# Performance work log

Measured on AMD Instinct MI355X. Metric: run time of the kernel, lower is better.

Reference implementation:

```python
import jax, jax.numpy as jnp
import numpy as np

N_NODES = 50000


def _gcn_conv(x, W, b, src, dst, n):
    # PyG GCNConv: h = x @ W, symmetric-normalized aggregation, then + bias.
    h = x @ W  # [N, out]
    deg = jax.ops.segment_sum(jnp.ones_like(dst, dtype=h.dtype), dst, num_segments=n)
    dinv = jnp.where(deg > 0, jax.lax.rsqrt(jnp.maximum(deg, 1e-12)), 0.0)
    norm = dinv[src] * dinv[dst]  # [E]
    msg = h[src] * norm[:, None]  # gather + scale, [E, out]
    out = jax.ops.segment_sum(msg, dst, num_segments=n)
    return out + b


def setup_inputs() -> dict:
    key = jax.random.key(0)
    ks = jax.random.split(key, 8)
    d_in, d_h, d_out = 256, 256, 128
    E = 800000
    x = jax.random.normal(ks[0], (N_NODES, d_in), dtype=jnp.float32)
    edge_index = jax.random.randint(ks[1], (2, E), 0, N_NODES, dtype=jnp.int64)
    def glorot(k, shape):
        lim = np.sqrt(6.0 / (shape[0] + shape[1]))
        return jax.random.uniform(k, shape, jnp.float32, -lim, lim)
    return {
        "x": x,
        "edge_index": edge_index,
        "W1": glorot(ks[2], (d_in, d_h)), "b1": jnp.zeros((d_h,), jnp.float32),
        "W2": glorot(ks[3], (d_h, d_h)), "b2": jnp.zeros((d_h,), jnp.float32),
        "W3": glorot(ks[4], (d_h, d_out)), "b3": jnp.zeros((d_out,), jnp.float32),
    }


def reference(x, edge_index, W1, b1, W2, b2, W3, b3):
    n = x.shape[0]
    # add self-loops once (PyG GCNConv default add_self_loops=True)
    loop = jnp.arange(n, dtype=edge_index.dtype)
    src = jnp.concatenate([edge_index[0], loop])
    dst = jnp.concatenate([edge_index[1], loop])
    h = _gcn_conv(x, W1, b1, src, dst, n)
    h = jax.nn.relu(h)  # dropout is identity in eval mode
    h = _gcn_conv(h, W2, b2, src, dst, n)
    h = jax.nn.relu(h)
    h = _gcn_conv(h, W3, b3, src, dst, n)
    return h
```

## Files before the change

kernel.cpp:

```cpp
#include <hip/hip_runtime.h>
#include <stdint.h>

typedef short v8s __attribute__((ext_vector_type(8)));
typedef float v4f __attribute__((ext_vector_type(4)));
typedef float v2f __attribute__((ext_vector_type(2)));

__device__ inline float bf2f(unsigned short h) {
    union { unsigned u; float f; } c; c.u = ((unsigned)h) << 16; return c.f;
}
__device__ inline unsigned short f2bf(float f) {
    union { float f; unsigned u; } c; c.f = f;
    unsigned u = c.u;
    unsigned r = (u + 0x7FFFu + ((u >> 16) & 1u)) >> 16;
    return (unsigned short)r;
}
__device__ inline void gl_lds16(const unsigned short* g, unsigned short* l) {
    __builtin_amdgcn_global_load_lds(
        (const __attribute__((address_space(1))) unsigned int*)(g),
        (__attribute__((address_space(3))) unsigned int*)(l), 16, 0, 0);
}

__global__ void k_pre1(const int* __restrict__ dst, int E,
                       int* __restrict__ cnt, int* __restrict__ seq,
                       const float* __restrict__ x, unsigned short* __restrict__ A,
                       int n, int mpad,
                       const float* __restrict__ W1, const float* __restrict__ W2,
                       const float* __restrict__ W3, unsigned short* __restrict__ Wt,
                       int gE, int gX) {
    int b = blockIdx.x;
    if (b < gE) {
        int e = b * 256 + threadIdx.x;
        if (e < E) seq[e] = atomicAdd(&cnt[dst[e]], 1);
    } else if (b < gE + gX) {
        int g = (b - gE) * 256 + threadIdx.x;
        int total = mpad * 64;
        if (g >= total) return;
        int row = g >> 6;
        float4 v;
        if (row < n) v = ((const float4*)x)[(size_t)g];
        else v = make_float4(0.f, 0.f, 0.f, 0.f);
        ushort4 o;
        o.x = f2bf(v.x); o.y = f2bf(v.y); o.z = f2bf(v.z); o.w = f2bf(v.w);
        ((ushort4*)A)[(size_t)g] = o;
    } else {
        int idx = (b - gE - gX) * 256 + threadIdx.x;
        const float* W; int base, N;
        if (idx < 65536)       { W = W1; base = 0;      N = 256; }
        else if (idx < 131072) { W = W2; base = 65536;  N = 256; }
        else                   { W = W3; base = 131072; N = 128; }
        int loc = idx - base;
        int nn = loc >> 8;
        int k = loc & 255;
        Wt[idx] = f2bf(W[(size_t)k * N + nn]);
    }
}

__global__ void k_scan1(const int* __restrict__ cnt, int n, int* __restrict__ incl,
                        int* __restrict__ bsum) {
    __shared__ int sm[256];
    int t = threadIdx.x;
    int i = blockIdx.x * 256 + t;
    int v = (i < n) ? cnt[i] : 0;
    sm[t] = v; __syncthreads();
    for (int off = 1; off < 256; off <<= 1) {
        int add = (t >= off) ? sm[t - off] : 0;
        __syncthreads();
        sm[t] += add;
        __syncthreads();
    }
    if (i < n) incl[i] = sm[t];
    if (t == 255) bsum[blockIdx.x] = sm[255];
}

__global__ void k_scan23(const int* __restrict__ cnt, int n,
                         const int* __restrict__ bsum,
                         int* __restrict__ rs, float* __restrict__ dinv) {
    __shared__ int red[256];
    int t = threadIdx.x;
    int acc = 0;
    for (int j = t; j < (int)blockIdx.x; j += 256) acc += bsum[j];
    red[t] = acc; __syncthreads();
    for (int s = 128; s > 0; s >>= 1) {
        if (t < s) red[t] += red[t + s];
        __syncthreads();
    }
    int boff = red[0];
    int i = blockIdx.x * 256 + t;
    if (i < n) {
        int c = cnt[i];
        rs[i] = rs[i] + boff - c;
        dinv[i] = rsqrtf((float)(c + 1));
    }
}

__global__ void k_scatter2(const int* __restrict__ src, const int* __restrict__ dst,
                           const int* __restrict__ seq, int E,
                           const int* __restrict__ rs, int* __restrict__ col) {
    int e = blockIdx.x * 256 + threadIdx.x;
    if (e < E) col[rs[dst[e]] + seq[e]] = src[e];
}

__launch_bounds__(256, 3)
__global__ void k_gemm(const unsigned short* __restrict__ A,
                       const unsigned short* __restrict__ Wt,
                       unsigned short* __restrict__ Hs,
                       const float* __restrict__ dinv, int n, int N) {
    __shared__ unsigned short sA[2][128 * 32];
    __shared__ unsigned short sB[2][128 * 32];
    const int t = threadIdx.x;
    const int lane = t & 63;
    const int wave = t >> 6;
    const int wm = wave >> 1, wn = wave & 1;
    const int m0 = blockIdx.x * 128;
    const int n0 = blockIdx.y * 128;

    v4f acc[4][4];
#pragma unroll
    for (int i = 0; i < 4; i++)
#pragma unroll
        for (int j = 0; j < 4; j++)
#pragma unroll
            for (int r = 0; r < 4; r++) acc[i][j][r] = 0.f;

    const int c0 = t, c1 = t + 256;
    const int r0 = c0 >> 2, kc0 = (c0 & 3) * 8;
    const int r1 = c1 >> 2, kc1 = (c1 & 3) * 8;
    const size_t aBase0 = (size_t)(m0 + r0) * 256 + kc0;
    const size_t aBase1 = (size_t)(m0 + r1) * 256 + kc1;
    const size_t bBase0 = (size_t)(n0 + r0) * 256 + kc0;
    const size_t bBase1 = (size_t)(n0 + r1) * 256 + kc1;

    const int q = lane >> 4;
    const int lm = lane & 15;

    gl_lds16(A + aBase0, &sA[0][c0 * 8]);
    gl_lds16(A + aBase1, &sA[0][c1 * 8]);
    gl_lds16(Wt + bBase0, &sB[0][c0 * 8]);
    gl_lds16(Wt + bBase1, &sB[0][c1 * 8]);

    for (int k0 = 0; k0 < 256; k0 += 32) {
        const int cur = (k0 >> 5) & 1;
        __syncthreads();
        if (k0 < 224) {
            const int nxt = cur ^ 1;
            gl_lds16(A + aBase0 + k0 + 32, &sA[nxt][c0 * 8]);
            gl_lds16(A + aBase1 + k0 + 32, &sA[nxt][c1 * 8]);
            gl_lds16(Wt + bBase0 + k0 + 32, &sB[nxt][c0 * 8]);
            gl_lds16(Wt + bBase1 + k0 + 32, &sB[nxt][c1 * 8]);
        }

        v8s afr[4], bfr[4];
#pragma unroll
        for (int i = 0; i < 4; i++) {
            int r = wm * 64 + i * 16 + lm;
            afr[i] = *(const v8s*)&sA[cur][r * 32 + q * 8];
        }
#pragma unroll
        for (int j = 0; j < 4; j++) {
            int nn = wn * 64 + j * 16 + lm;
            bfr[j] = *(const v8s*)&sB[cur][nn * 32 + q * 8];
        }
#pragma unroll
        for (int i = 0; i < 4; i++)
#pragma unroll
            for (int j = 0; j < 4; j++)
                acc[i][j] = __builtin_amdgcn_mfma_f32_16x16x32_bf16(afr[i], bfr[j],
                                                                    acc[i][j], 0, 0, 0);
    }

#pragma unroll
    for (int i = 0; i < 4; i++) {
        int mbase = m0 + wm * 64 + i * 16 + q * 4;
#pragma unroll
        for (int r = 0; r < 4; r++) {
            int m = mbase + r;
            float s = (m < n) ? dinv[m] : 0.f;
#pragma unroll
            for (int j = 0; j < 4; j++) {
                int colI = n0 + wn * 64 + j * 16 + lm;
                Hs[(size_t)m * N + colI] = f2bf(acc[i][j][r] * s);
            }
        }
    }
}

template <int D, bool RELU, bool F32OUT>
__launch_bounds__(256, 8)
__global__ void k_agg(const unsigned short* __restrict__ Hs,
                      const int* __restrict__ rs, const int* __restrict__ cnt,
                      const int* __restrict__ col, const float* __restrict__ dinv,
                      const float* __restrict__ bias,
                      unsigned short* __restrict__ outb, float* __restrict__ outf,
                      int n, int nzero) {
    constexpr int LPN = D / 8;
    constexpr int NPG = 64 / LPN;
    const int lane = threadIdx.x & 63;
    const int i = blockIdx.x * 4 + (threadIdx.x >> 6);
    if (i >= n) return;
    const int g = lane / LPN;
    const int cl = lane % LPN;

    v2f acc[4];
#pragma unroll
    for (int k = 0; k < 4; k++) acc[k] = (v2f){0.f, 0.f};

    auto accq = [&](unsigned u, int k) {
        union { unsigned uu; float f; } lo, hi;
        lo.uu = u << 16;
        hi.uu = u & 0xffff0000u;
        v2f t; t[0] = lo.f; t[1] = hi.f;
        acc[k] += t;
    };
    auto acc16 = [&](uint4 q) { accq(q.x, 0); accq(q.y, 1); accq(q.z, 2); accq(q.w, 3); };

    const unsigned short* base = Hs + cl * 8;
    const int s = rs[i], deg = cnt[i];
    const int T = deg + 1;
    const int Tpad = (T + NPG - 1) & ~(NPG - 1);

    for (int b = 0; b < Tpad; b += 64) {
        int t = b + lane;
        int v;
        if (t == 0) v = i;
        else if (t <= deg) v = col[s + t - 1];
        else v = nzero;
        int lim = min(64, Tpad - b);
        int t2 = 0;
        for (; t2 + 4 * NPG <= lim; t2 += 4 * NPG) {
            int c0 = __shfl(v, t2 + 0 * NPG + g);
            int c1 = __shfl(v, t2 + 1 * NPG + g);
            int c2 = __shfl(v, t2 + 2 * NPG + g);
            int c3 = __shfl(v, t2 + 3 * NPG + g);
            uint4 q0 = *(const uint4*)(base + (size_t)c0 * D);
            uint4 q1 = *(const uint4*)(base + (size_t)c1 * D);
            uint4 q2 = *(const uint4*)(base + (size_t)c2 * D);
            uint4 q3 = *(const uint4*)(base + (size_t)c3 * D);
            acc16(q0); acc16(q1); acc16(q2); acc16(q3);
        }
        for (; t2 + NPG <= lim; t2 += NPG) {
            int c0 = __shfl(v, t2 + g);
            uint4 q0 = *(const uint4*)(base + (size_t)c0 * D);
            acc16(q0);
        }
    }

#pragma unroll
    for (int off = LPN; off < 64; off <<= 1) {
#pragma unroll
        for (int k = 0; k < 4; k++) {
            acc[k][0] += __shfl_xor(acc[k][0], off);
            acc[k][1] += __shfl_xor(acc[k][1], off);
        }
    }

    if (g == 0) {
        float di = dinv[i];
        float o[8];
#pragma unroll
        for (int k = 0; k < 4; k++) {
            o[2 * k + 0] = di * acc[k][0] + bias[cl * 8 + 2 * k + 0];
            o[2 * k + 1] = di * acc[k][1] + bias[cl * 8 + 2 * k + 1];
        }
        if (RELU) {
#pragma unroll
            for (int k = 0; k < 8; k++) o[k] = fmaxf(o[k], 0.f);
        }
        if constexpr (F32OUT) {
            float* p = outf + (size_t)i * D + cl * 8;
            *(float4*)p = make_float4(o[0], o[1], o[2], o[3]);
            *(float4*)(p + 4) = make_float4(o[4], o[5], o[6], o[7]);
        } else {
            uint4 q;
            q.x = ((unsigned)f2bf(o[1]) << 16) | f2bf(o[0]);
            q.y = ((unsigned)f2bf(o[3]) << 16) | f2bf(o[2]);
            q.z = ((unsigned)f2bf(o[5]) << 16) | f2bf(o[4]);
            q.w = ((unsigned)f2bf(o[7]) << 16) | f2bf(o[6]);
            *(uint4*)(outb + (size_t)i * D + cl * 8) = q;
        }
    }
}

extern "C" void kernel_launch(void* const* d_in, const int* in_sizes, int n_in,
                              void* d_out, int out_size, void* d_ws, size_t ws_size,
                              hipStream_t stream) {
    const float* x  = (const float*)d_in[0];
    const int*   ei = (const int*)d_in[1];
    const float* W1 = (const float*)d_in[2];
    const float* b1 = (const float*)d_in[3];
    const float* W2 = (const float*)d_in[4];
    const float* b2 = (const float*)d_in[5];
    const float* W3 = (const float*)d_in[6];
    const float* b3 = (const float*)d_in[7];

    const int n = in_sizes[0] / 256;
    const int E = in_sizes[1] / 2;
    const int mpad = ((n + 127) / 128) * 128;

    char* ws = (char*)d_ws;
    size_t off = 0;
    auto alloc = [&](size_t bytes) -> void* {
        void* p = ws + off;
        off += (bytes + 255) & ~(size_t)255;
        return p;
    };
    int* cnt      = (int*)alloc((size_t)n * 4);
    int* rs       = (int*)alloc((size_t)n * 4);
    float* dinv   = (float*)alloc((size_t)n * 4);
    int* bsum     = (int*)alloc(256 * 4);
    int* seq      = (int*)alloc((size_t)E * 4);
    int* col      = (int*)alloc((size_t)E * 4);
    unsigned short* Wt = (unsigned short*)alloc((size_t)163840 * 2);
    unsigned short* W1t = Wt;
    unsigned short* W2t = Wt + 65536;
    unsigned short* W3t = Wt + 131072;
    unsigned short* bufA = (unsigned short*)alloc((size_t)mpad * 256 * 2);
    unsigned short* bufB = (unsigned short*)alloc((size_t)mpad * 256 * 2);
    (void)ws_size; (void)n_in; (void)out_size;

    const int* srcp = ei;
    const int* dstp = ei + E;
    const int gE = (E + 255) / 256;
    const int gN = (n + 255) / 256;
    const int gX = (mpad * 64 + 255) / 256;
    const int gW = 640;

    hipMemsetAsync(cnt, 0, (size_t)n * 4, stream);

    k_pre1<<<gE + gX + gW, 256, 0, stream>>>(dstp, E, cnt, seq, x, bufA, n, mpad,
                                             W1, W2, W3, Wt, gE, gX);
    k_scan1<<<gN, 256, 0, stream>>>(cnt, n, rs, bsum);
    k_scan23<<<gN, 256, 0, stream>>>(cnt, n, bsum, rs, dinv);
    k_scatter2<<<gE, 256, 0, stream>>>(srcp, dstp, seq, E, rs, col);

    const int gAgg = (n + 3) / 4;
    dim3 gg1(mpad / 128, 2);
    k_gemm<<<gg1, 256, 0, stream>>>(bufA, W1t, bufB, dinv, n, 256);
    k_agg<256, true, false><<<gAgg, 256, 0, stream>>>(bufB, rs, cnt, col, dinv, b1,
                                                      bufA, nullptr, n, n);
    k_gemm<<<gg1, 256, 0, stream>>>(bufA, W2t, bufB, dinv, n, 256);
    k_agg<256, true, false><<<gAgg, 256, 0, stream>>>(bufB, rs, cnt, col, dinv, b2,
                                                      bufA, nullptr, n, n);
    dim3 gg3(mpad / 128, 1);
    k_gemm<<<gg3, 256, 0, stream>>>(bufA, W3t, bufB, dinv, n, 128);
    k_agg<128, false, true><<<gAgg, 256, 0, stream>>>(bufB, rs, cnt, col, dinv, b3,
                                                      nullptr, (float*)d_out, n, n);
}
```

Measured before the change: 364.3 us.

## Shrink GEMM tile to 64x128, drop LDS double buffering, raise occupancy

The GEMM block tile shrinks from 128x128 to 64x128, with each wave computing a 64x32 slice. The two-stage LDS double buffer is replaced by a single buffer guarded by two barriers per k-step, and launch bounds rise to 6 blocks per SM. The aim is to double the grid size and raise occupancy so latency is hidden by more resident waves rather than by software prefetch. The cost is lower data reuse per block (each W tile is fetched twice as often), extra barriers, and no overlap of loads with MFMA inside a block.

```diff
diff --git a/kernel.cpp b/kernel.cpp
--- a/kernel.cpp
+++ b/kernel.cpp
@@ -100,84 +100,70 @@
     if (e < E) col[rs[dst[e]] + seq[e]] = src[e];
 }
 
-__launch_bounds__(256, 3)
+__launch_bounds__(256, 6)
 __global__ void k_gemm(const unsigned short* __restrict__ A,
                        const unsigned short* __restrict__ Wt,
                        unsigned short* __restrict__ Hs,
                        const float* __restrict__ dinv, int n, int N) {
-    __shared__ unsigned short sA[2][128 * 32];
-    __shared__ unsigned short sB[2][128 * 32];
+    __shared__ unsigned short sA[64 * 32];
+    __shared__ unsigned short sB[128 * 32];
     const int t = threadIdx.x;
     const int lane = t & 63;
-    const int wave = t >> 6;
-    const int wm = wave >> 1, wn = wave & 1;
-    const int m0 = blockIdx.x * 128;
+    const int wn = t >> 6;
+    const int m0 = blockIdx.x * 64;
     const int n0 = blockIdx.y * 128;
 
-    v4f acc[4][4];
+    v4f acc[4][2];
 #pragma unroll
     for (int i = 0; i < 4; i++)
 #pragma unroll
-        for (int j = 0; j < 4; j++)
+        for (int j = 0; j < 2; j++)
 #pragma unroll
             for (int r = 0; r < 4; r++) acc[i][j][r] = 0.f;
 
     const int c0 = t, c1 = t + 256;
-    const int r0 = c0 >> 2, kc0 = (c0 & 3) * 8;
-    const int r1 = c1 >> 2, kc1 = (c1 & 3) * 8;
-    const size_t aBase0 = (size_t)(m0 + r0) * 256 + kc0;
-    const size_t aBase1 = (size_t)(m0 + r1) * 256 + kc1;
-    const size_t bBase0 = (size_t)(n0 + r0) * 256 + kc0;
-    const size_t bBase1 = (size_t)(n0 + r1) * 256 + kc1;
+    const int rA = c0 >> 2, kA = (c0 & 3) * 8;
+    const int rB0 = c0 >> 2, kB0 = (c0 & 3) * 8;
+    const int rB1 = c1 >> 2, kB1 = (c1 & 3) * 8;
+    const size_t aBase  = (size_t)(m0 + rA) * 256 + kA;
+    const size_t bBase0 = (size_t)(n0 + rB0) * 256 + kB0;
+    const size_t bBase1 = (size_t)(n0 + rB1) * 256 + kB1;
 
     const int q = lane >> 4;
     const int lm = lane & 15;
 
-    gl_lds16(A + aBase0, &sA[0][c0 * 8]);
-    gl_lds16(A + aBase1, &sA[0][c1 * 8]);
-    gl_lds16(Wt + bBase0, &sB[0][c0 * 8]);
-    gl_lds16(Wt + bBase1, &sB[0][c1 * 8]);
-
     for (int k0 = 0; k0 < 256; k0 += 32) {
-        const int cur = (k0 >> 5) & 1;
-        __syncthreads();
-        if (k0 < 224) {
-            const int nxt = cur ^ 1;
-            gl_lds16(A + aBase0 + k0 + 32, &sA[nxt][c0 * 8]);
-            gl_lds16(A + aBase1 + k0 + 32, &sA[nxt][c1 * 8]);
-            gl_lds16(Wt + bBase0 + k0 + 32, &sB[nxt][c0 * 8]);
-            gl_lds16(Wt + bBase1 + k0 + 32, &sB[nxt][c1 * 8]);
-        }
-
-        v8s afr[4], bfr[4];
-#pragma unroll
-        for (int i = 0; i < 4; i++) {
-            int r = wm * 64 + i * 16 + lm;
-            afr[i] = *(const v8s*)&sA[cur][r * 32 + q * 8];
-        }
-#pragma unroll
-        for (int j = 0; j < 4; j++) {
-            int nn = wn * 64 + j * 16 + lm;
-            bfr[j] = *(const v8s*)&sB[cur][nn * 32 + q * 8];
-        }
+        __syncthreads();
+        gl_lds16(A + aBase + k0, &sA[c0 * 8]);
+        gl_lds16(Wt + bBase0 + k0, &sB[c0 * 8]);
+        gl_lds16(Wt + bBase1 + k0, &sB[c1 * 8]);
+        __syncthreads();
+
+        v8s afr[4], bfr[2];
 #pragma unroll
         for (int i = 0; i < 4; i++)
-#pragma unroll
-            for (int j = 0; j < 4; j++)
+            afr[i] = *(const v8s*)&sA[(i * 16 + lm) * 32 + q * 8];
+#pragma unroll
+        for (int j = 0; j < 2; j++)
+            bfr[j] = *(const v8s*)&sB[(wn * 32 + j * 16 + lm) * 32 + q * 8];
+#pragma unroll
+        for (int i = 0; i < 4; i++)
+#pragma unroll
+            for (int j = 0; j < 2; j++)
                 acc[i][j] = __builtin_amdgcn_mfma_f32_16x16x32_bf16(afr[i], bfr[j],
                                                                     acc[i][j], 0, 0, 0);
     }
 
 #pragma unroll
     for (int i = 0; i < 4; i++) {
-        int mbase = m0 + wm * 64 + i * 16 + q * 4;
+        int mbase = m0 + i * 16 + q * 4;
 #pragma unroll
         for (int r = 0; r < 4; r++) {
             int m = mbase + r;
             float s = (m < n) ? dinv[m] : 0.f;
 #pragma unroll
-            for (int j = 0; j < 4; j++) {
-                int colI = n0 + wn * 64 + j * 16 + lm;
+            for (int j = 0; j < 2; j++) {
+                int colI = n0 + wn * 32 + j * 16 + lm;
                 Hs[(size_t)m * N + colI] = f2bf(acc[i][j][r] * s);
             }
         }
@@ -333,14 +319,15 @@
     k_scatter2<<<gE, 256, 0, stream>>>(srcp, dstp, seq, E, rs, col);
 
     const int gAgg = (n + 3) / 4;
-    dim3 gg1(mpad / 128, 2);
+    const int nmb64 = mpad / 64;
+    dim3 gg1(nmb64, 2);
     k_gemm<<<gg1, 256, 0, stream>>>(bufA, W1t, bufB, dinv, n, 256);
     k_agg<256, true, false><<<gAgg, 256, 0, stream>>>(bufB, rs, cnt, col, dinv, b1,
                                                       bufA, nullptr, n, n);
     k_gemm<<<gg1, 256, 0, stream>>>(bufA, W2t, bufB, dinv, n, 256);
     k_agg<256, true, false><<<gAgg, 256, 0, stream>>>(bufB, rs, cnt, col, dinv, b2,
                                                       bufA, nullptr, n, n);
-    dim3 gg3(mpad / 128, 1);
+    dim3 gg3(nmb64, 1);
     k_gemm<<<gg3, 256, 0, stream>>>(bufA, W3t, bufB, dinv, n, 128);
     k_agg<128, false, true><<<gAgg, 256, 0, stream>>>(bufB, rs, cnt, col, dinv, b3,
                                                       nullptr, (float*)d_out, n, n);
```

New measurement: 361.8 us. Within noise of the previous version (-0.7%).
